# Performance work log

Measured on AMD Instinct MI355X. Metric: run time of the kernel, lower is better.

The kernel has to match this reference:

```python
import jax, jax.numpy as jnp
import numpy as np

EPS = 1e-6
V_LO, V_HI = 0.95, 1.05
N_NODES = 100000
N_EDGES = 3200000


def setup_inputs() -> dict:
    key = jax.random.key(0)
    k1, k2, k3, k4 = jax.random.split(key, 4)
    node_features = jax.random.normal(k1, (N_NODES, 4), dtype=jnp.float32)
    edge_index = jax.random.randint(k2, (2, N_EDGES), 0, N_NODES, dtype=jnp.int64)
    edge_probs = jax.random.uniform(k3, (N_EDGES,), dtype=jnp.float32)
    edge_params = jax.random.uniform(k4, (N_EDGES, 2), dtype=jnp.float32)
    return {
        "node_features": node_features,
        "edge_index": edge_index,
        "edge_probs": edge_probs,
        "edge_params": edge_params,
    }


def reference(node_features, edge_index, edge_probs, edge_params):
    n_nodes = node_features.shape[0]
    src = edge_index[0]
    dst = edge_index[1]

    # power flow on each edge, computed from the SRC node voltage magnitude
    v_mag_src = jnp.sqrt(node_features[src, 0] ** 2 + node_features[src, 1] ** 2)  # [E]
    v2 = v_mag_src ** 2
    p_e = v2 / (edge_params[:, 0] + EPS) * edge_probs  # [E]
    q_e = v2 / (edge_params[:, 1] + EPS) * edge_probs  # [E]

    # each edge contributes to both endpoints; self-loops contribute only once
    self_loop = src == dst
    p_e_dst = jnp.where(self_loop, 0.0, p_e)
    q_e_dst = jnp.where(self_loop, 0.0, q_e)

    p_flow = (jax.ops.segment_sum(p_e, src, num_segments=n_nodes)
              + jax.ops.segment_sum(p_e_dst, dst, num_segments=n_nodes))  # [N]
    q_flow = (jax.ops.segment_sum(q_e, src, num_segments=n_nodes)
              + jax.ops.segment_sum(q_e_dst, dst, num_segments=n_nodes))  # [N]

    p_load = node_features[:, 2]
    q_load = node_features[:, 3]
    power_balance_loss = jnp.mean((p_load + p_flow) ** 2 + (q_load + q_flow) ** 2)

    # voltage magnitude box constraint
    v_mag = jnp.sqrt(node_features[:, 0] ** 2 + node_features[:, 1] ** 2)
    lower_viol = jax.nn.relu(V_LO - v_mag)
    upper_viol = jax.nn.relu(v_mag - V_HI)
    voltage_loss = jnp.mean(lower_viol ** 2 + upper_viol ** 2)

    return power_balance_loss + voltage_loss
```

## Files before the change

kernel.cpp:

```cpp
#include <hip/hip_runtime.h>

#define EPS 1e-6f
#define V_LO 0.95f
#define V_HI 1.05f

#define BIN_ELEMS 20480
#define TPB 1024
#define MAX_SPLIT 51
#define BATCH 4

typedef float f32x2 __attribute__((ext_vector_type(2)));

__global__ void pf_v2_kernel(const float4* __restrict__ nf4,
                             float* __restrict__ v2tab, int n_nodes) {
    int i = blockIdx.x * blockDim.x + threadIdx.x;
    if (i < n_nodes) {
        float4 f = nf4[i];
        v2tab[i] = f.x * f.x + f.y * f.y;
    }
}

__global__ __launch_bounds__(TPB) void pf_edge_scan(
    const float* __restrict__ v2tab,
    const int* __restrict__ ei,
    const float* __restrict__ probs,
    const float* __restrict__ params,
    float* __restrict__ partial,
    int n_edges, int n_nodes, int nbins, int per_chunk)
{
    extern __shared__ float lds[];
    int bin  = blockIdx.x % nbins;
    int slot = blockIdx.x / nbins;
    int node_base = bin * BIN_ELEMS;

    for (int i = threadIdx.x; i < 2 * BIN_ELEMS; i += TPB)
        lds[i] = 0.0f;
    __syncthreads();

    int e0 = slot * per_chunk;
    int e1 = min(e0 + per_chunk, n_edges);

    for (int e = e0 + threadIdx.x * BATCH; e < e1; e += TPB * BATCH) {
        if (e + BATCH <= e1) {
            int4   s4  = *reinterpret_cast<const int4*>(&ei[e]);
            int4   d4  = *reinterpret_cast<const int4*>(&ei[n_edges + e]);
            float4 pb4 = *reinterpret_cast<const float4*>(&probs[e]);
            float4 prA = *reinterpret_cast<const float4*>(&params[(size_t)e * 2]);
            float4 prB = *reinterpret_cast<const float4*>(&params[(size_t)e * 2 + 4]);

            float v2_0 = v2tab[s4.x];
            float v2_1 = v2tab[s4.y];
            float v2_2 = v2tab[s4.z];
            float v2_3 = v2tab[s4.w];

            #pragma unroll
            for (int k = 0; k < BATCH; ++k) {
                int   src  = (k == 0) ? s4.x : (k == 1) ? s4.y : (k == 2) ? s4.z : s4.w;
                int   dst  = (k == 0) ? d4.x : (k == 1) ? d4.y : (k == 2) ? d4.z : d4.w;
                float prob = (k == 0) ? pb4.x : (k == 1) ? pb4.y : (k == 2) ? pb4.z : pb4.w;
                float prx  = (k == 0) ? prA.x : (k == 1) ? prA.z : (k == 2) ? prB.x : prB.z;
                float pry  = (k == 0) ? prA.y : (k == 1) ? prA.w : (k == 2) ? prB.y : prB.w;
                float v2   = (k == 0) ? v2_0 : (k == 1) ? v2_1 : (k == 2) ? v2_2 : v2_3;

                unsigned ls = (unsigned)(src - node_base);
                unsigned ld = (unsigned)(dst - node_base);
                bool cs = ls < (unsigned)BIN_ELEMS;
                bool cd = (ld < (unsigned)BIN_ELEMS) & (src != dst);
                if (cs | cd) {
                    float pe = v2 * prob * __builtin_amdgcn_rcpf(prx + EPS);
                    float qe = v2 * prob * __builtin_amdgcn_rcpf(pry + EPS);
                    if (cs) {
                        atomicAdd(&lds[2 * ls],     pe);
                        atomicAdd(&lds[2 * ls + 1], qe);
                    }
                    if (cd) {
                        atomicAdd(&lds[2 * ld],     pe);
                        atomicAdd(&lds[2 * ld + 1], qe);
                    }
                }
            }
        } else {
            for (int t = e; t < e1; ++t) {
                int src = ei[t];
                int dst = ei[n_edges + t];
                unsigned ls = (unsigned)(src - node_base);
                unsigned ld = (unsigned)(dst - node_base);
                bool cs = ls < (unsigned)BIN_ELEMS;
                bool cd = (ld < (unsigned)BIN_ELEMS) & (src != dst);
                if (cs | cd) {
                    float v2 = v2tab[src];
                    float pe = v2 * probs[t] * __builtin_amdgcn_rcpf(params[(size_t)t * 2] + EPS);
                    float qe = v2 * probs[t] * __builtin_amdgcn_rcpf(params[(size_t)t * 2 + 1] + EPS);
                    if (cs) { atomicAdd(&lds[2 * ls], pe); atomicAdd(&lds[2 * ls + 1], qe); }
                    if (cd) { atomicAdd(&lds[2 * ld], pe); atomicAdd(&lds[2 * ld + 1], qe); }
                }
            }
        }
    }
    __syncthreads();

    int lim = min(BIN_ELEMS, n_nodes - node_base);
    float* out = partial + (size_t)slot * n_nodes * 2 + (size_t)node_base * 2;
    const f32x2* lds2 = reinterpret_cast<const f32x2*>(lds);
    f32x2* out2 = reinterpret_cast<f32x2*>(out);
    for (int i = threadIdx.x; i < lim; i += TPB)
        __builtin_nontemporal_store(lds2[i], &out2[i]);
}

__global__ void pf_node_kernel(const float* __restrict__ nf,
                               const float* __restrict__ partial,
                               float* __restrict__ acc,
                               int n_nodes, int split) {
    int i = blockIdx.x * blockDim.x + threadIdx.x;
    float c = 0.0f;
    if (i < n_nodes) {
        float4 f = *reinterpret_cast<const float4*>(&nf[(size_t)i * 4]);
        float p = f.z, q = f.w;
        const f32x2* pp = reinterpret_cast<const f32x2*>(partial) + i;
        for (int s = 0; s < split; ++s) {
            f32x2 fl = __builtin_nontemporal_load(&pp[(size_t)s * n_nodes]);
            p += fl.x;
            q += fl.y;
        }
        float vmag = sqrtf(f.x * f.x + f.y * f.y);
        float lv = fmaxf(V_LO - vmag, 0.0f);
        float uv = fmaxf(vmag - V_HI, 0.0f);
        c = p * p + q * q + lv * lv + uv * uv;
    }
    #pragma unroll
    for (int off = 32; off > 0; off >>= 1)
        c += __shfl_down(c, off);
    __shared__ float wsum[4];
    int lane = threadIdx.x & 63;
    int wid  = threadIdx.x >> 6;
    if (lane == 0) wsum[wid] = c;
    __syncthreads();
    if (threadIdx.x == 0) {
        float s = 0.0f;
        int nw = blockDim.x >> 6;
        for (int w = 0; w < nw; ++w) s += wsum[w];
        atomicAdd(acc, s);
    }
}

__global__ void pf_finalize_kernel(const float* __restrict__ acc,
                                   float* __restrict__ out,
                                   float inv_n) {
    out[0] = acc[0] * inv_n;
}

extern "C" void kernel_launch(void* const* d_in, const int* in_sizes, int n_in,
                              void* d_out, int out_size, void* d_ws, size_t ws_size,
                              hipStream_t stream) {
    const float* nf     = (const float*)d_in[0];
    const int*   ei     = (const int*)d_in[1];
    const float* probs  = (const float*)d_in[2];
    const float* params = (const float*)d_in[3];

    int n_nodes = in_sizes[0] / 4;
    int n_edges = in_sizes[2];

    float* acc   = (float*)d_ws;
    float* v2tab = (float*)((char*)d_ws + 256);
    size_t v2_bytes = ((size_t)n_nodes * sizeof(float) + 255) & ~(size_t)255;
    float* partial = (float*)((char*)d_ws + 256 + v2_bytes);

    size_t slot_bytes = (size_t)n_nodes * 2 * sizeof(float);
    int split = (int)((ws_size - 256 - v2_bytes) / slot_bytes);
    if (split > MAX_SPLIT) split = MAX_SPLIT;
    if (split < 1) split = 1;

    int nbins = (n_nodes + BIN_ELEMS - 1) / BIN_ELEMS;
    int per_chunk = (n_edges + split - 1) / split;
    per_chunk = (per_chunk + 3) & ~3;

    size_t lds_bytes = (size_t)(2 * BIN_ELEMS) * sizeof(float);
    (void)hipFuncSetAttribute((const void*)pf_edge_scan,
                              hipFuncAttributeMaxDynamicSharedMemorySize,
                              (int)lds_bytes);

    (void)hipMemsetAsync(d_ws, 0, 256, stream);

    pf_v2_kernel<<<(n_nodes + 255) / 256, 256, 0, stream>>>(
        (const float4*)nf, v2tab, n_nodes);

    pf_edge_scan<<<nbins * split, TPB, lds_bytes, stream>>>(
        v2tab, ei, probs, params, partial, n_edges, n_nodes, nbins, per_chunk);

    int nblocks = (n_nodes + 255) / 256;
    pf_node_kernel<<<nblocks, 256, 0, stream>>>(nf, partial, acc, n_nodes, split);

    pf_finalize_kernel<<<1, 1, 0, stream>>>(acc, (float*)d_out,
                                            1.0f / (float)n_nodes);
}
```

Baseline: 124.8 us.

## Precompute per-edge p/q as packed bf16 once, shrink edge-scan reads

Adds a pre-pass kernel that computes each edge's p and q flow once and stores them as a packed bf16 pair in one u32. The binned edge scan, which runs once per node bin (5 bins), then reads src, dst and the 4-byte pq word instead of probs, 8-byte params and a gathered v2. This cuts repeated per-bin traffic and gather work. The node reduction kernel is also changed to handle two nodes per thread with float4 partial loads. The trade-offs are an extra kernel plus a pq buffer that reduces the workspace left for split slots, and bf16 rounding of per-edge flows, which lowers accumulated precision.

```diff
diff --git a/kernel.cpp b/kernel.cpp
--- a/kernel.cpp
+++ b/kernel.cpp
@@ -10,6 +10,7 @@
 #define BATCH 4
 
 typedef float f32x2 __attribute__((ext_vector_type(2)));
+typedef unsigned int u32;
 
 __global__ void pf_v2_kernel(const float4* __restrict__ nf4,
                              float* __restrict__ v2tab, int n_nodes) {
@@ -20,11 +21,65 @@
     }
 }
 
-__global__ __launch_bounds__(TPB) void pf_edge_scan(
+__device__ __forceinline__ u32 bf16_hi(float x) {
+    u32 b = __float_as_uint(x);
+    b += 0x7FFFu + ((b >> 16) & 1u);
+    return b >> 16;
+}
+
+__global__ __launch_bounds__(256) void pf_pq_kernel(
     const float* __restrict__ v2tab,
     const int* __restrict__ ei,
     const float* __restrict__ probs,
     const float* __restrict__ params,
+    u32* __restrict__ pq, int n_edges)
+{
+    int e = (blockIdx.x * blockDim.x + threadIdx.x) * BATCH;
+    if (e >= n_edges) return;
+    if (e + BATCH <= n_edges) {
+        int4   s4  = *reinterpret_cast<const int4*>(&ei[e]);
+        float4 pb4 = *reinterpret_cast<const float4*>(&probs[e]);
+        float4 prA = *reinterpret_cast<const float4*>(&params[(size_t)e * 2]);
+        float4 prB = *reinterpret_cast<const float4*>(&params[(size_t)e * 2 + 4]);
+        float v2_0 = v2tab[s4.x];
+        float v2_1 = v2tab[s4.y];
+        float v2_2 = v2tab[s4.z];
+        float v2_3 = v2tab[s4.w];
+        uint4 out;
+        {
+            float pe = v2_0 * pb4.x * __builtin_amdgcn_rcpf(prA.x + EPS);
+            float qe = v2_0 * pb4.x * __builtin_amdgcn_rcpf(prA.y + EPS);
+            out.x = bf16_hi(pe) | (bf16_hi(qe) << 16);
+        }
+        {
+            float pe = v2_1 * pb4.y * __builtin_amdgcn_rcpf(prA.z + EPS);
+            float qe = v2_1 * pb4.y * __builtin_amdgcn_rcpf(prA.w + EPS);
+            out.y = bf16_hi(pe) | (bf16_hi(qe) << 16);
+        }
+        {
+            float pe = v2_2 * pb4.z * __builtin_amdgcn_rcpf(prB.x + EPS);
+            float qe = v2_2 * pb4.z * __builtin_amdgcn_rcpf(prB.y + EPS);
+            out.z = bf16_hi(pe) | (bf16_hi(qe) << 16);
+        }
+        {
+            float pe = v2_3 * pb4.w * __builtin_amdgcn_rcpf(prB.z + EPS);
+            float qe = v2_3 * pb4.w * __builtin_amdgcn_rcpf(prB.w + EPS);
+            out.w = bf16_hi(pe) | (bf16_hi(qe) << 16);
+        }
+        *reinterpret_cast<uint4*>(&pq[e]) = out;
+    } else {
+        for (int t = e; t < n_edges; ++t) {
+            float v2 = v2tab[ei[t]];
+            float pe = v2 * probs[t] * __builtin_amdgcn_rcpf(params[(size_t)t * 2] + EPS);
+            float qe = v2 * probs[t] * __builtin_amdgcn_rcpf(params[(size_t)t * 2 + 1] + EPS);
+            pq[t] = bf16_hi(pe) | (bf16_hi(qe) << 16);
+        }
+    }
+}
+
+__global__ __launch_bounds__(TPB) void pf_edge_scan(
+    const int* __restrict__ ei,
+    const u32* __restrict__ pq,
     float* __restrict__ partial,
     int n_edges, int n_nodes, int nbins, int per_chunk)
 {
@@ -42,33 +97,23 @@
 
     for (int e = e0 + threadIdx.x * BATCH; e < e1; e += TPB * BATCH) {
         if (e + BATCH <= e1) {
-            int4   s4  = *reinterpret_cast<const int4*>(&ei[e]);
-            int4   d4  = *reinterpret_cast<const int4*>(&ei[n_edges + e]);
-            float4 pb4 = *reinterpret_cast<const float4*>(&probs[e]);
-            float4 prA = *reinterpret_cast<const float4*>(&params[(size_t)e * 2]);
-            float4 prB = *reinterpret_cast<const float4*>(&params[(size_t)e * 2 + 4]);
-
-            float v2_0 = v2tab[s4.x];
-            float v2_1 = v2tab[s4.y];
-            float v2_2 = v2tab[s4.z];
-            float v2_3 = v2tab[s4.w];
+            int4  s4 = *reinterpret_cast<const int4*>(&ei[e]);
+            int4  d4 = *reinterpret_cast<const int4*>(&ei[n_edges + e]);
+            uint4 w4 = *reinterpret_cast<const uint4*>(&pq[e]);
 
             #pragma unroll
             for (int k = 0; k < BATCH; ++k) {
-                int   src  = (k == 0) ? s4.x : (k == 1) ? s4.y : (k == 2) ? s4.z : s4.w;
-                int   dst  = (k == 0) ? d4.x : (k == 1) ? d4.y : (k == 2) ? d4.z : d4.w;
-                float prob = (k == 0) ? pb4.x : (k == 1) ? pb4.y : (k == 2) ? pb4.z : pb4.w;
-                float prx  = (k == 0) ? prA.x : (k == 1) ? prA.z : (k == 2) ? prB.x : prB.z;
-                float pry  = (k == 0) ? prA.y : (k == 1) ? prA.w : (k == 2) ? prB.y : prB.w;
-                float v2   = (k == 0) ? v2_0 : (k == 1) ? v2_1 : (k == 2) ? v2_2 : v2_3;
+                int src = (k == 0) ? s4.x : (k == 1) ? s4.y : (k == 2) ? s4.z : s4.w;
+                int dst = (k == 0) ? d4.x : (k == 1) ? d4.y : (k == 2) ? d4.z : d4.w;
+                u32 w   = (k == 0) ? w4.x : (k == 1) ? w4.y : (k == 2) ? w4.z : w4.w;
 
                 unsigned ls = (unsigned)(src - node_base);
                 unsigned ld = (unsigned)(dst - node_base);
                 bool cs = ls < (unsigned)BIN_ELEMS;
                 bool cd = (ld < (unsigned)BIN_ELEMS) & (src != dst);
                 if (cs | cd) {
-                    float pe = v2 * prob * __builtin_amdgcn_rcpf(prx + EPS);
-                    float qe = v2 * prob * __builtin_amdgcn_rcpf(pry + EPS);
+                    float pe = __uint_as_float(w << 16);
+                    float qe = __uint_as_float(w & 0xFFFF0000u);
                     if (cs) {
                         atomicAdd(&lds[2 * ls],     pe);
                         atomicAdd(&lds[2 * ls + 1], qe);
@@ -83,14 +128,14 @@
             for (int t = e; t < e1; ++t) {
                 int src = ei[t];
                 int dst = ei[n_edges + t];
+                u32 w   = pq[t];
                 unsigned ls = (unsigned)(src - node_base);
                 unsigned ld = (unsigned)(dst - node_base);
                 bool cs = ls < (unsigned)BIN_ELEMS;
                 bool cd = (ld < (unsigned)BIN_ELEMS) & (src != dst);
                 if (cs | cd) {
-                    float v2 = v2tab[src];
-                    float pe = v2 * probs[t] * __builtin_amdgcn_rcpf(params[(size_t)t * 2] + EPS);
-                    float qe = v2 * probs[t] * __builtin_amdgcn_rcpf(params[(size_t)t * 2 + 1] + EPS);
+                    float pe = __uint_as_float(w << 16);
+                    float qe = __uint_as_float(w & 0xFFFF0000u);
                     if (cs) { atomicAdd(&lds[2 * ls], pe); atomicAdd(&lds[2 * ls + 1], qe); }
                     if (cd) { atomicAdd(&lds[2 * ld], pe); atomicAdd(&lds[2 * ld + 1], qe); }
                 }
@@ -101,31 +146,40 @@
 
     int lim = min(BIN_ELEMS, n_nodes - node_base);
     float* out = partial + (size_t)slot * n_nodes * 2 + (size_t)node_base * 2;
-    const f32x2* lds2 = reinterpret_cast<const f32x2*>(lds);
-    f32x2* out2 = reinterpret_cast<f32x2*>(out);
-    for (int i = threadIdx.x; i < lim; i += TPB)
-        __builtin_nontemporal_store(lds2[i], &out2[i]);
+    for (int i = threadIdx.x; i < lim; i += TPB) {
+        f32x2 vv; vv.x = lds[2 * i]; vv.y = lds[2 * i + 1];
+        __builtin_nontemporal_store(vv, &reinterpret_cast<f32x2*>(out)[i]);
+    }
 }
 
 __global__ void pf_node_kernel(const float* __restrict__ nf,
                                const float* __restrict__ partial,
                                float* __restrict__ acc,
                                int n_nodes, int split) {
-    int i = blockIdx.x * blockDim.x + threadIdx.x;
+    int i2 = (blockIdx.x * blockDim.x + threadIdx.x) * 2;
     float c = 0.0f;
-    if (i < n_nodes) {
-        float4 f = *reinterpret_cast<const float4*>(&nf[(size_t)i * 4]);
-        float p = f.z, q = f.w;
-        const f32x2* pp = reinterpret_cast<const f32x2*>(partial) + i;
+    if (i2 < n_nodes) {
+        bool two = (i2 + 1) < n_nodes;
+        float4 fa = *reinterpret_cast<const float4*>(&nf[(size_t)i2 * 4]);
+        float4 fb = two ? *reinterpret_cast<const float4*>(&nf[(size_t)(i2 + 1) * 4])
+                        : make_float4(0, 0, 0, 0);
+        float pa = fa.z, qa = fa.w, pb = fb.z, qb = fb.w;
+        const float* pp = partial + (size_t)i2 * 2;
         for (int s = 0; s < split; ++s) {
-            f32x2 fl = __builtin_nontemporal_load(&pp[(size_t)s * n_nodes]);
-            p += fl.x;
-            q += fl.y;
-        }
-        float vmag = sqrtf(f.x * f.x + f.y * f.y);
+            float4 fl = *reinterpret_cast<const float4*>(&pp[(size_t)s * n_nodes * 2]);
+            pa += fl.x; qa += fl.y;
+            pb += fl.z; qb += fl.w;
+        }
+        float vmag = sqrtf(fa.x * fa.x + fa.y * fa.y);
         float lv = fmaxf(V_LO - vmag, 0.0f);
         float uv = fmaxf(vmag - V_HI, 0.0f);
-        c = p * p + q * q + lv * lv + uv * uv;
+        c = pa * pa + qa * qa + lv * lv + uv * uv;
+        if (two) {
+            float vmag2 = sqrtf(fb.x * fb.x + fb.y * fb.y);
+            float lv2 = fmaxf(V_LO - vmag2, 0.0f);
+            float uv2 = fmaxf(vmag2 - V_HI, 0.0f);
+            c += pb * pb + qb * qb + lv2 * lv2 + uv2 * uv2;
+        }
     }
     #pragma unroll
     for (int off = 32; off > 0; off >>= 1)
@@ -144,8 +198,7 @@
 }
 
 __global__ void pf_finalize_kernel(const float* __restrict__ acc,
-                                   float* __restrict__ out,
-                                   float inv_n) {
+                                   float* __restrict__ out, float inv_n) {
     out[0] = acc[0] * inv_n;
 }
 
@@ -163,10 +216,13 @@
     float* acc   = (float*)d_ws;
     float* v2tab = (float*)((char*)d_ws + 256);
     size_t v2_bytes = ((size_t)n_nodes * sizeof(float) + 255) & ~(size_t)255;
-    float* partial = (float*)((char*)d_ws + 256 + v2_bytes);
+    u32*   pq    = (u32*)((char*)d_ws + 256 + v2_bytes);
+    size_t pq_bytes = ((size_t)n_edges * sizeof(u32) + 255) & ~(size_t)255;
+    float* partial = (float*)((char*)d_ws + 256 + v2_bytes + pq_bytes);
 
     size_t slot_bytes = (size_t)n_nodes * 2 * sizeof(float);
-    int split = (int)((ws_size - 256 - v2_bytes) / slot_bytes);
+    long long avail = (long long)ws_size - 256 - (long long)v2_bytes - (long long)pq_bytes;
+    int split = (avail > 0) ? (int)(avail / (long long)slot_bytes) : 0;
     if (split > MAX_SPLIT) split = MAX_SPLIT;
     if (split < 1) split = 1;
 
@@ -184,10 +240,14 @@
     pf_v2_kernel<<<(n_nodes + 255) / 256, 256, 0, stream>>>(
         (const float4*)nf, v2tab, n_nodes);
 
+    int pq_blocks = (n_edges + 256 * BATCH - 1) / (256 * BATCH);
+    pf_pq_kernel<<<pq_blocks, 256, 0, stream>>>(
+        v2tab, ei, probs, params, pq, n_edges);
+
     pf_edge_scan<<<nbins * split, TPB, lds_bytes, stream>>>(
-        v2tab, ei, probs, params, partial, n_edges, n_nodes, nbins, per_chunk);
-
-    int nblocks = (n_nodes + 255) / 256;
+        ei, pq, partial, n_edges, n_nodes, nbins, per_chunk);
+
+    int nblocks = (n_nodes / 2 + 255) / 256;
     pf_node_kernel<<<nblocks, 256, 0, stream>>>(nf, partial, acc, n_nodes, split);
 
     pf_finalize_kernel<<<1, 1, 0, stream>>>(acc, (float*)d_out,
```

Measured after the change: 132.4 us. 1.06x slower.
